# Kernel tuning notes

Measured on AMD Instinct MI355X. Metric: run time of the kernel, lower is better.

The kernel has to match this reference:

```python
import jax, jax.numpy as jnp
import numpy as np

IN_CH, OUT_CH, K, DIL = 64, 128, 3, 8

def setup_inputs() -> dict:
    key = jax.random.key(0)
    k1, k2, k3 = jax.random.split(key, 3)
    x = jax.random.normal(k1, (16, IN_CH, 128, 128), dtype=jnp.float32)
    # xavier_normal-like init for W
    fan_in, fan_out = IN_CH * K * K, OUT_CH * K * K
    std = (2.0 / (fan_in + fan_out)) ** 0.5
    W = jax.random.normal(k2, (OUT_CH, IN_CH, K, K), dtype=jnp.float32) * std
    b = jax.random.normal(k3, (OUT_CH,), dtype=jnp.float32)
    return {"x": x, "W": W, "b": b}

def reference(x, W, b):
    pad = DIL * (K // 2)  # circular halo so output spatial size == input
    xp = jnp.pad(x, ((0, 0), (0, 0), (pad, pad), (pad, pad)), mode="wrap")
    y = jax.lax.conv_general_dilated(
        xp, W,
        window_strides=(1, 1),
        padding="VALID",
        rhs_dilation=(DIL, DIL),
        dimension_numbers=("NCHW", "OIHW", "NCHW"),
    )
    return y + b[None, :, None, None]
```

## Files before the change

### kernel.cpp

```cpp
#include <hip/hip_runtime.h>

#define IN_CH 64
#define OUT_CH 128
#define HW 128
#define KTAPS 9
#define ROWB 16384

typedef __bf16 bf16x8 __attribute__((ext_vector_type(8)));
typedef float f32x16 __attribute__((ext_vector_type(16)));
typedef float f32x4 __attribute__((ext_vector_type(4)));

__device__ __forceinline__ unsigned f2bf(float f) {
    unsigned u = __builtin_bit_cast(unsigned, f);
    return (u + 0x7FFFu + ((u >> 16) & 1u)) >> 16;
}

__device__ __forceinline__ unsigned cvt_pk_bf16(float lo, float hi) {
    unsigned r;
    asm("v_cvt_pk_bf16_f32 %0, %1, %2" : "=v"(r) : "v"(lo), "v"(hi));
    return r;
}

__device__ __forceinline__ int swz(int r) { return ((r ^ (r >> 3)) & 7) << 4; }

__global__ void wprep_kernel(const float* __restrict__ W, unsigned short* __restrict__ Wl) {
    int i = blockIdx.x * blockDim.x + threadIdx.x;
    if (i >= OUT_CH * IN_CH * KTAPS) return;
    int p  = i / 36864;
    int r  = i % 36864;
    int t  = r >> 12;
    int r2 = r & 4095;
    int m  = r2 >> 11;
    int ks = (r2 >> 9) & 3;
    int l  = (r2 >> 3) & 63;
    int e  = r2 & 7;
    int oc = p * 64 + m * 32 + (l & 31);
    int ic = ks * 16 + (l >> 5) * 8 + e;
    int kh = t / 3, kw = t % 3;
    Wl[i] = (unsigned short)f2bf(W[((oc * IN_CH + ic) * 3 + kh) * 3 + kw]);
}

__global__ __launch_bounds__(512, 6) void conv_kernel_f(
    const float* __restrict__ x, const unsigned short* __restrict__ Wl,
    const float* __restrict__ bias, float* __restrict__ y)
{
    __shared__ __align__(16) unsigned char xsB[3 * ROWB];

    int bid = blockIdx.x;
    int sb  = (bid & 7) * 256 + (bid >> 3);
    int n = sb >> 7, h = sb & 127;
    int tid = threadIdx.x;
    int wid = tid >> 6, lane = tid & 63;

    #pragma unroll
    for (int g = 0; g < 3; ++g) {
        int q   = g * 512 + tid;
        int w4  = q & 31;
        int ic4 = (q >> 5) & 15;
        int kh  = q >> 9;
        int srow = (h + kh * 8 + 120) & 127;
        const float* xp = x + (((n * IN_CH + ic4 * 4) * HW + srow) * HW + w4 * 4);
        f32x4 v[4];
        #pragma unroll
        for (int j = 0; j < 4; ++j)
            v[j] = *reinterpret_cast<const f32x4*>(xp + j * (HW * HW));
        #pragma unroll
        for (int j2 = 0; j2 < 4; ++j2) {
            int w = w4 * 4 + j2;
            uint2 pk;
            pk.x = cvt_pk_bf16(v[0][j2], v[1][j2]);
            pk.y = cvt_pk_bf16(v[2][j2], v[3][j2]);
            *reinterpret_cast<uint2*>(xsB + kh * ROWB + ((w * 128 + ic4 * 8) ^ swz(w))) = pk;
        }
    }
    __syncthreads();

    int wr = wid >> 1, wc = wid & 1;
    int l31 = lane & 31, lhi = lane >> 5;
    int p = wr >> 1, m = wr & 1;

    const bf16x8* Ab = reinterpret_cast<const bf16x8*>(Wl)
                     + p * (9 * 512) + m * 256 + lane;

    f32x16 acc[2];
    #pragma unroll
    for (int bq = 0; bq < 2; ++bq)
        #pragma unroll
        for (int r = 0; r < 16; ++r) acc[bq][r] = 0.0f;

    #pragma unroll
    for (int t = 0; t < 9; ++t) {
        bf16x8 aCur[4];
        #pragma unroll
        for (int ks = 0; ks < 4; ++ks) aCur[ks] = Ab[t * 512 + ks * 64];

        int kh = t / 3, kw = t % 3;
        int xc0 = (wc * 64 + l31 + 8 * kw - 8) & 127;
        int xc1 = (xc0 + 32) & 127;
        int b0base = kh * ROWB + xc0 * 128 + lhi * 16, s0 = swz(xc0);
        int b1base = kh * ROWB + xc1 * 128 + lhi * 16, s1 = swz(xc1);
        #pragma unroll
        for (int ks = 0; ks < 4; ++ks) {
            bf16x8 b0 = *reinterpret_cast<const bf16x8*>(xsB + ((b0base + ks * 32) ^ s0));
            bf16x8 b1 = *reinterpret_cast<const bf16x8*>(xsB + ((b1base + ks * 32) ^ s1));
            acc[0] = __builtin_amdgcn_mfma_f32_32x32x16_bf16(aCur[ks], b0, acc[0], 0, 0, 0);
            acc[1] = __builtin_amdgcn_mfma_f32_32x32x16_bf16(aCur[ks], b1, acc[1], 0, 0, 0);
        }
    }

    int outbase = (n * OUT_CH) * HW * HW + h * HW;
    #pragma unroll
    for (int bq = 0; bq < 2; ++bq) {
        int wcol = wc * 64 + bq * 32 + l31;
        #pragma unroll
        for (int reg = 0; reg < 16; ++reg) {
            int oc = wr * 32 + (reg & 3) + 8 * (reg >> 2) + 4 * lhi;
            y[outbase + oc * HW * HW + wcol] = acc[bq][reg] + bias[oc];
        }
    }
}

extern "C" void kernel_launch(void* const* d_in, const int* in_sizes, int n_in,
                              void* d_out, int out_size, void* d_ws, size_t ws_size,
                              hipStream_t stream) {
    const float* x = (const float*)d_in[0];
    const float* W = (const float*)d_in[1];
    const float* b = (const float*)d_in[2];
    float* y = (float*)d_out;

    unsigned short* Wl = (unsigned short*)d_ws;

    hipLaunchKernelGGL(wprep_kernel, dim3((OUT_CH * IN_CH * KTAPS + 255) / 256), dim3(256), 0, stream, W, Wl);
    hipLaunchKernelGGL(conv_kernel_f, dim3(16 * HW), dim3(512), 0, stream, x, Wl, b, y);
}
```

Baseline: 63.69 us.

## Process four dilated rows per block with rolling LDS row buffer

Each block now computes four output rows spaced by the dilation (hb, hb+8, hb+16, hb+24) and keeps a four-slot ring of staged bf16 input rows in LDS, so each new output row loads only one new input row instead of three. Bias is hoisted into registers, and the grid shrinks from 2048 to 512 blocks. This cuts redundant global reads and fp32-to-bf16 conversion work. In exchange, LDS use per block rises, occupancy bounds drop, and there are fewer blocks to spread across CUs. The per-row staging also sits serially next to MFMA work with a barrier per row.

After: 115.8 us. +81.8%, slower.

```diff
diff --git a/kernel.cpp b/kernel.cpp
--- a/kernel.cpp
+++ b/kernel.cpp
@@ -40,25 +40,33 @@
     Wl[i] = (unsigned short)f2bf(W[((oc * IN_CH + ic) * 3 + kh) * 3 + kw]);
 }
 
-__global__ __launch_bounds__(512, 6) void conv_kernel_f(
+__global__ __launch_bounds__(512, 4) void conv_kernel_f(
     const float* __restrict__ x, const unsigned short* __restrict__ Wl,
     const float* __restrict__ bias, float* __restrict__ y)
 {
-    __shared__ __align__(16) unsigned char xsB[3 * ROWB];
+    __shared__ __align__(16) unsigned char xs[4 * ROWB];
 
     int bid = blockIdx.x;
-    int sb  = (bid & 7) * 256 + (bid >> 3);
-    int n = sb >> 7, h = sb & 127;
+    int n   = (bid & 7) | (((bid >> 8) & 1) << 3);
+    int rem = (bid >> 3) & 31;
+    int hb  = (rem & 7) + ((rem >> 3) << 5);
     int tid = threadIdx.x;
     int wid = tid >> 6, lane = tid & 63;
 
+    int wr = wid >> 1, wc = wid & 1;
+    int l31 = lane & 31, lhi = lane >> 5;
+    int p = wr >> 1, m = wr & 1;
+
+    const bf16x8* Ab = reinterpret_cast<const bf16x8*>(Wl)
+                     + p * (9 * 512) + m * 256 + lane;
+
+    float bv[16];
     #pragma unroll
-    for (int g = 0; g < 3; ++g) {
-        int q   = g * 512 + tid;
-        int w4  = q & 31;
-        int ic4 = (q >> 5) & 15;
-        int kh  = q >> 9;
-        int srow = (h + kh * 8 + 120) & 127;
+    for (int reg = 0; reg < 16; ++reg)
+        bv[reg] = bias[wr * 32 + (reg & 3) + 8 * (reg >> 2) + 4 * lhi];
+
+    auto STAGE = [&](int slot, int srow) {
+        int w4 = tid & 31, ic4 = tid >> 5;
         const float* xp = x + (((n * IN_CH + ic4 * 4) * HW + srow) * HW + w4 * 4);
         f32x4 v[4];
         #pragma unroll
@@ -70,53 +78,59 @@
             uint2 pk;
             pk.x = cvt_pk_bf16(v[0][j2], v[1][j2]);
             pk.y = cvt_pk_bf16(v[2][j2], v[3][j2]);
-            *reinterpret_cast<uint2*>(xsB + kh * ROWB + ((w * 128 + ic4 * 8) ^ swz(w))) = pk;
+            *reinterpret_cast<uint2*>(xs + slot * ROWB + ((w * 128 + ic4 * 8) ^ swz(w))) = pk;
         }
-    }
+    };
+
+    STAGE(0, (hb + 120) & 127);
+    STAGE(1, hb);
+    STAGE(2, (hb + 8) & 127);
     __syncthreads();
 
-    int wr = wid >> 1, wc = wid & 1;
-    int l31 = lane & 31, lhi = lane >> 5;
-    int p = wr >> 1, m = wr & 1;
-
-    const bf16x8* Ab = reinterpret_cast<const bf16x8*>(Wl)
-                     + p * (9 * 512) + m * 256 + lane;
-
     f32x16 acc[2];
-    #pragma unroll
-    for (int bq = 0; bq < 2; ++bq)
-        #pragma unroll
-        for (int r = 0; r < 16; ++r) acc[bq][r] = 0.0f;
 
     #pragma unroll
-    for (int t = 0; t < 9; ++t) {
-        bf16x8 aCur[4];
+    for (int j = 0; j < 4; ++j) {
+        if (j < 3) STAGE((j + 3) & 3, (hb + 8 * j + 16) & 127);
+
         #pragma unroll
-        for (int ks = 0; ks < 4; ++ks) aCur[ks] = Ab[t * 512 + ks * 64];
+        for (int bq = 0; bq < 2; ++bq)
+            #pragma unroll
+            for (int r = 0; r < 16; ++r) acc[bq][r] = 0.0f;
 
-        int kh = t / 3, kw = t % 3;
-        int xc0 = (wc * 64 + l31 + 8 * kw - 8) & 127;
-        int xc1 = (xc0 + 32) & 127;
-        int b0base = kh * ROWB + xc0 * 128 + lhi * 16, s0 = swz(xc0);
-        int b1base = kh * ROWB + xc1 * 128 + lhi * 16, s1 = swz(xc1);
         #pragma unroll
-        for (int ks = 0; ks < 4; ++ks) {
-            bf16x8 b0 = *reinterpret_cast<const bf16x8*>(xsB + ((b0base + ks * 32) ^ s0));
-            bf16x8 b1 = *reinterpret_cast<const bf16x8*>(xsB + ((b1base + ks * 32) ^ s1));
-            acc[0] = __builtin_amdgcn_mfma_f32_32x32x16_bf16(aCur[ks], b0, acc[0], 0, 0, 0);
-            acc[1] = __builtin_amdgcn_mfma_f32_32x32x16_bf16(aCur[ks], b1, acc[1], 0, 0, 0);
+        for (int t = 0; t < 9; ++t) {
+            bf16x8 aCur[4];
+            #pragma unroll
+            for (int ks = 0; ks < 4; ++ks) aCur[ks] = Ab[t * 512 + ks * 64];
+
+            int kh = t / 3, kw = t % 3;
+            int sbase = ((j + kh) & 3) * ROWB;
+            int xc0 = (wc * 64 + l31 + 8 * kw - 8) & 127;
+            int xc1 = (xc0 + 32) & 127;
+            int b0base = sbase + xc0 * 128 + lhi * 16, s0 = swz(xc0);
+            int b1base = sbase + xc1 * 128 + lhi * 16, s1 = swz(xc1);
+            #pragma unroll
+            for (int ks = 0; ks < 4; ++ks) {
+                bf16x8 b0 = *reinterpret_cast<const bf16x8*>(xs + ((b0base + ks * 32) ^ s0));
+                bf16x8 b1 = *reinterpret_cast<const bf16x8*>(xs + ((b1base + ks * 32) ^ s1));
+                acc[0] = __builtin_amdgcn_mfma_f32_32x32x16_bf16(aCur[ks], b0, acc[0], 0, 0, 0);
+                acc[1] = __builtin_amdgcn_mfma_f32_32x32x16_bf16(aCur[ks], b1, acc[1], 0, 0, 0);
+            }
         }
-    }
 
-    int outbase = (n * OUT_CH) * HW * HW + h * HW;
-    #pragma unroll
-    for (int bq = 0; bq < 2; ++bq) {
-        int wcol = wc * 64 + bq * 32 + l31;
+        int outbase = (n * OUT_CH) * HW * HW + (hb + 8 * j) * HW;
         #pragma unroll
-        for (int reg = 0; reg < 16; ++reg) {
-            int oc = wr * 32 + (reg & 3) + 8 * (reg >> 2) + 4 * lhi;
-            y[outbase + oc * HW * HW + wcol] = acc[bq][reg] + bias[oc];
+        for (int bq = 0; bq < 2; ++bq) {
+            int wcol = wc * 64 + bq * 32 + l31;
+            #pragma unroll
+            for (int reg = 0; reg < 16; ++reg) {
+                int oc = wr * 32 + (reg & 3) + 8 * (reg >> 2) + 4 * lhi;
+                y[outbase + oc * HW * HW + wcol] = acc[bq][reg] + bv[reg];
+            }
         }
+
+        __syncthreads();
     }
 }
 
@@ -131,5 +145,5 @@
     unsigned short* Wl = (unsigned short*)d_ws;
 
     hipLaunchKernelGGL(wprep_kernel, dim3((OUT_CH * IN_CH * KTAPS + 255) / 256), dim3(256), 0, stream, W, Wl);
-    hipLaunchKernelGGL(conv_kernel_f, dim3(16 * HW), dim3(512), 0, stream, x, Wl, b, y);
+    hipLaunchKernelGGL(conv_kernel_f, dim3(512), dim3(512), 0, stream, x, Wl, b, y);
 }
```

## Pipeline input row staging with MFMA taps per kernel row

Applied to the files above, without the earlier changes.

Splits the single up-front staging of three input rows into per-row stages. The global load of the next row is issued before the MFMA taps of the current row run, so load latency overlaps compute, with a barrier after each stage. It also batches the LDS B-fragment reads before the MFMAs, raises wave priority around the MFMA block, and lowers the occupancy hint from 6 to 4 blocks per CU. The extra barriers and the extra registers held for prefetched rows may reduce occupancy.

Result: slower. 71.67 us (+12.5%).

```diff
diff --git a/kernel.cpp b/kernel.cpp
--- a/kernel.cpp
+++ b/kernel.cpp
@@ -40,7 +40,7 @@
     Wl[i] = (unsigned short)f2bf(W[((oc * IN_CH + ic) * 3 + kh) * 3 + kw]);
 }
 
-__global__ __launch_bounds__(512, 6) void conv_kernel_f(
+__global__ __launch_bounds__(512, 4) void conv_kernel_f(
     const float* __restrict__ x, const unsigned short* __restrict__ Wl,
     const float* __restrict__ bias, float* __restrict__ y)
 {
@@ -52,29 +52,6 @@
     int tid = threadIdx.x;
     int wid = tid >> 6, lane = tid & 63;
 
-    #pragma unroll
-    for (int g = 0; g < 3; ++g) {
-        int q   = g * 512 + tid;
-        int w4  = q & 31;
-        int ic4 = (q >> 5) & 15;
-        int kh  = q >> 9;
-        int srow = (h + kh * 8 + 120) & 127;
-        const float* xp = x + (((n * IN_CH + ic4 * 4) * HW + srow) * HW + w4 * 4);
-        f32x4 v[4];
-        #pragma unroll
-        for (int j = 0; j < 4; ++j)
-            v[j] = *reinterpret_cast<const f32x4*>(xp + j * (HW * HW));
-        #pragma unroll
-        for (int j2 = 0; j2 < 4; ++j2) {
-            int w = w4 * 4 + j2;
-            uint2 pk;
-            pk.x = cvt_pk_bf16(v[0][j2], v[1][j2]);
-            pk.y = cvt_pk_bf16(v[2][j2], v[3][j2]);
-            *reinterpret_cast<uint2*>(xsB + kh * ROWB + ((w * 128 + ic4 * 8) ^ swz(w))) = pk;
-        }
-    }
-    __syncthreads();
-
     int wr = wid >> 1, wc = wid & 1;
     int l31 = lane & 31, lhi = lane >> 5;
     int p = wr >> 1, m = wr & 1;
@@ -82,31 +59,78 @@
     const bf16x8* Ab = reinterpret_cast<const bf16x8*>(Wl)
                      + p * (9 * 512) + m * 256 + lane;
 
+    int w4 = tid & 31, ic4 = tid >> 5;
+    const float* xg = x + ((n * IN_CH + ic4 * 4) * HW) * HW + w4 * 4;
+
+    auto LOADROW = [&](int kh, f32x4 v[4]) {
+        int srow = (h + kh * 8 + 120) & 127;
+        const float* xp = xg + srow * HW;
+        #pragma unroll
+        for (int j = 0; j < 4; ++j)
+            v[j] = *reinterpret_cast<const f32x4*>(xp + j * (HW * HW));
+    };
+    auto WRITEROW = [&](int kh, const f32x4 v[4]) {
+        #pragma unroll
+        for (int j2 = 0; j2 < 4; ++j2) {
+            int c = w4 * 4 + j2;
+            uint2 pk;
+            pk.x = cvt_pk_bf16(v[0][j2], v[1][j2]);
+            pk.y = cvt_pk_bf16(v[2][j2], v[3][j2]);
+            *reinterpret_cast<uint2*>(xsB + kh * ROWB + ((c * 128 + ic4 * 8) ^ swz(c))) = pk;
+        }
+    };
+
     f32x16 acc[2];
     #pragma unroll
     for (int bq = 0; bq < 2; ++bq)
         #pragma unroll
         for (int r = 0; r < 16; ++r) acc[bq][r] = 0.0f;
 
-    #pragma unroll
-    for (int t = 0; t < 9; ++t) {
-        bf16x8 aCur[4];
+    auto TAPS = [&](int kh) {
         #pragma unroll
-        for (int ks = 0; ks < 4; ++ks) aCur[ks] = Ab[t * 512 + ks * 64];
+        for (int kw = 0; kw < 3; ++kw) {
+            int t = kh * 3 + kw;
+            bf16x8 aCur[4];
+            #pragma unroll
+            for (int ks = 0; ks < 4; ++ks) aCur[ks] = Ab[t * 512 + ks * 64];
+            int xc0 = (wc * 64 + l31 + 8 * kw - 8) & 127;
+            int xc1 = (xc0 + 32) & 127;
+            int b0base = kh * ROWB + xc0 * 128 + lhi * 16, s0 = swz(xc0);
+            int b1base = kh * ROWB + xc1 * 128 + lhi * 16, s1 = swz(xc1);
+            bf16x8 b[8];
+            #pragma unroll
+            for (int ks = 0; ks < 4; ++ks) {
+                b[ks]     = *reinterpret_cast<const bf16x8*>(xsB + ((b0base + ks * 32) ^ s0));
+                b[4 + ks] = *reinterpret_cast<const bf16x8*>(xsB + ((b1base + ks * 32) ^ s1));
+            }
+            __builtin_amdgcn_s_setprio(1);
+            #pragma unroll
+            for (int ks = 0; ks < 4; ++ks) {
+                acc[0] = __builtin_amdgcn_mfma_f32_32x32x16_bf16(aCur[ks], b[ks],     acc[0], 0, 0, 0);
+                acc[1] = __builtin_amdgcn_mfma_f32_32x32x16_bf16(aCur[ks], b[4 + ks], acc[1], 0, 0, 0);
+            }
+            __builtin_amdgcn_s_setprio(0);
+        }
+    };
 
-        int kh = t / 3, kw = t % 3;
-        int xc0 = (wc * 64 + l31 + 8 * kw - 8) & 127;
-        int xc1 = (xc0 + 32) & 127;
-        int b0base = kh * ROWB + xc0 * 128 + lhi * 16, s0 = swz(xc0);
-        int b1base = kh * ROWB + xc1 * 128 + lhi * 16, s1 = swz(xc1);
-        #pragma unroll
-        for (int ks = 0; ks < 4; ++ks) {
-            bf16x8 b0 = *reinterpret_cast<const bf16x8*>(xsB + ((b0base + ks * 32) ^ s0));
-            bf16x8 b1 = *reinterpret_cast<const bf16x8*>(xsB + ((b1base + ks * 32) ^ s1));
-            acc[0] = __builtin_amdgcn_mfma_f32_32x32x16_bf16(aCur[ks], b0, acc[0], 0, 0, 0);
-            acc[1] = __builtin_amdgcn_mfma_f32_32x32x16_bf16(aCur[ks], b1, acc[1], 0, 0, 0);
-        }
-    }
+    f32x4 v0[4], v1[4];
+    LOADROW(0, v0);
+    WRITEROW(0, v0);
+    __syncthreads();
+
+    LOADROW(1, v1);
+    __builtin_amdgcn_sched_barrier(0);
+    TAPS(0);
+    WRITEROW(1, v1);
+    __syncthreads();
+
+    LOADROW(2, v0);
+    __builtin_amdgcn_sched_barrier(0);
+    TAPS(1);
+    WRITEROW(2, v0);
+    __syncthreads();
+
+    TAPS(2);
 
     int outbase = (n * OUT_CH) * HW * HW + h * HW;
     #pragma unroll
```
